# Kernel tuning notes

Measured on AMD Instinct MI355X. Metric: run time of the kernel, lower is better.

The kernel has to match this reference:

```python
import jax, jax.numpy as jnp
import numpy as np

T, H, E, I, K = 4096, 2048, 8, 1408, 2


def setup_inputs() -> dict:
    key = jax.random.key(0)
    k1, k2, k3, k4 = jax.random.split(key, 4)
    x = jax.random.normal(k1, (T, H), dtype=jnp.float32)
    router_w = jax.random.normal(k2, (H, E), dtype=jnp.float32) * 0.02
    gate_up_proj = jax.random.normal(k3, (E, H, 2 * I), dtype=jnp.float32) * 0.02
    down_proj = jax.random.normal(k4, (E, I, H), dtype=jnp.float32) * 0.02
    return {"x": x, "router_w": router_w, "gate_up_proj": gate_up_proj, "down_proj": down_proj}


def _moe_forward(x, router_w, gate_up_proj, down_proj):
    # --- Router: softmax over experts, top-k selection (Qwen2-MoE style) ---
    logits = x @ router_w                                  # [T, E]
    probs = jax.nn.softmax(logits, axis=-1)
    topk_w, topk_idx = jax.lax.top_k(probs, K)             # [T, K]

    # --- Permute: replicate tokens per selected expert, stable-sort by expert id ---
    flat_eid = topk_idx.reshape(-1)                        # [T*K]
    rep_x = jnp.repeat(x, K, axis=0)                       # [T*K, H]
    sort_idx = jnp.argsort(flat_eid, stable=True)          # token permute (like ops.permute)
    perm_x = rep_x[sort_idx]                               # [T*K, H] grouped by expert
    perm_eid = flat_eid[sort_idx]                          # [T*K]

    # --- Grouped expert MLP (gate_up GEMM -> SiLU*up -> down GEMM) ---
    # Faithful to grouped-GEMM math; expressed as a fixed loop over E experts
    # with row masking to stay jit-compatible (no data-dependent shapes).
    out = jnp.zeros_like(perm_x)
    for e in range(E):
        gu = perm_x @ gate_up_proj[e]                      # [T*K, 2I]
        gate, up = gu[:, :I], gu[:, I:]
        h = (jax.nn.silu(gate) * up) @ down_proj[e]        # [T*K, H]
        out = out + jnp.where((perm_eid == e)[:, None], h, 0.0)

    # --- Unpermute + weighted combine over top-k ---
    inv_sort = jnp.argsort(sort_idx)                       # inverse permute mapping
    unperm = out[inv_sort].reshape(T, K, H)
    return jnp.einsum('tkh,tk->th', unperm, topk_w)        # [T, H]


def reference(x, router_w, gate_up_proj, down_proj):
    return _moe_forward(x, router_w, gate_up_proj, down_proj)
```

## Files before the change

### kernel.cpp

```cpp
#include <hip/hip_runtime.h>
#include <hip/hip_bf16.h>

#define T_TOK 4096
#define H_DIM 2048
#define E_NUM 8
#define I_DIM 1408
#define RTOT  8192
#define N1DIM 2816
#define MAXMT 40
#define MAXROWS 10752
#define NT1   11
#define NKT1  64
#define NKT2  44
#define G1_BLOCKS 440
#define GU_TILES 11264
#define DN_BLOCKS 2816
#define RT_BLOCKS 1024

#define BUF1U 16384
#define LDS1  131072

typedef __bf16 bf16x8 __attribute__((ext_vector_type(8)));
typedef float  floatx4 __attribute__((ext_vector_type(4)));
typedef unsigned short ushortx8 __attribute__((ext_vector_type(8)));

#define VMCNT(n) asm volatile("s_waitcnt vmcnt(" #n ")" ::: "memory")
#define LGK0() do { asm volatile("s_waitcnt lgkmcnt(0)" ::: "memory"); __builtin_amdgcn_sched_barrier(0); } while(0)

__device__ __forceinline__ unsigned short f2bf(float f) {
  union { float f; unsigned u; } v; v.f = f;
  unsigned r = v.u + 0x7FFFu + ((v.u >> 16) & 1u);
  return (unsigned short)(r >> 16);
}

__device__ __forceinline__ void async16(const void* g, void* l) {
  __builtin_amdgcn_global_load_lds(
      (__attribute__((address_space(1))) void*)(g),
      (__attribute__((address_space(3))) void*)(l), 16, 0, 0);
}

__global__ void prep_kernel(const float* __restrict__ W, unsigned short* __restrict__ W1T,
                            const float* __restrict__ x, const float* __restrict__ rw,
                            int* __restrict__ topk_idx, float* __restrict__ topk_w,
                            int* __restrict__ counts) {
  __shared__ unsigned short t[64][72];
  int bid = blockIdx.x;
  if (bid < RT_BLOCKS) {
    int wave = threadIdx.x >> 6, lane = threadIdx.x & 63;
    int tk = bid * 4 + wave;
    const float* xr = x + (size_t)tk * H_DIM;
    float acc[E_NUM];
#pragma unroll
    for (int e = 0; e < E_NUM; e++) acc[e] = 0.f;
    for (int h = lane; h < H_DIM; h += 64) {
      float xv = xr[h];
      const float* wr = rw + h * E_NUM;
#pragma unroll
      for (int e = 0; e < E_NUM; e++) acc[e] += xv * wr[e];
    }
#pragma unroll
    for (int e = 0; e < E_NUM; e++) {
      float v = acc[e];
#pragma unroll
      for (int s = 32; s > 0; s >>= 1) v += __shfl_xor(v, s, 64);
      acc[e] = v;
    }
    if (lane == 0) {
      float mx = acc[0];
#pragma unroll
      for (int e = 1; e < E_NUM; e++) mx = fmaxf(mx, acc[e]);
      float p[E_NUM], s = 0.f;
#pragma unroll
      for (int e = 0; e < E_NUM; e++) { p[e] = __expf(acc[e] - mx); s += p[e]; }
      float inv = 1.0f / s;
      int i0 = 0;
#pragma unroll
      for (int e = 1; e < E_NUM; e++) if (p[e] > p[i0]) i0 = e;
      int i1 = (i0 == 0) ? 1 : 0;
#pragma unroll
      for (int e = 0; e < E_NUM; e++) if (e != i0 && p[e] > p[i1]) i1 = e;
      topk_idx[tk * 2]     = i0;
      topk_idx[tk * 2 + 1] = i1;
      topk_w[tk * 2]       = p[i0] * inv;
      topk_w[tk * 2 + 1]   = p[i1] * inv;
      atomicAdd(&counts[i0], 1);
      atomicAdd(&counts[i1], 1);
    }
    return;
  }
  int b = bid - RT_BLOCKS;
  int kt = b & 31;
  int j  = (b >> 5) % 44;
  int e  = b / (32 * 44);
  int f4 = threadIdx.x & 15, kr = threadIdx.x >> 4;
  int up = f4 >> 3, cc = (f4 & 7) * 4;
  int src_col = (up ? I_DIM : 0) + 32 * j + cc;
  int lrow = 32 * (cc >> 4) + 16 * up + (cc & 15);
  const float* src = W + ((size_t)e * H_DIM + (size_t)kt * 64) * (2 * I_DIM) + src_col;
#pragma unroll
  for (int p = 0; p < 4; p++) {
    int k = kr + p * 16;
    float4 v = *(const float4*)(src + (size_t)k * (2 * I_DIM));
    t[lrow + 0][k] = f2bf(v.x);
    t[lrow + 1][k] = f2bf(v.y);
    t[lrow + 2][k] = f2bf(v.z);
    t[lrow + 3][k] = f2bf(v.w);
  }
  __syncthreads();
  int c = threadIdx.x & 15, nr = threadIdx.x >> 4;
  unsigned short* Op = W1T + ((size_t)e * N1DIM + 64 * j) * H_DIM + kt * 64;
#pragma unroll
  for (int p = 0; p < 4; p++) {
    int n = nr + p * 16;
    *(ushort4*)(Op + (size_t)n * H_DIM + c * 4) = *(const ushort4*)&t[n][c * 4];
  }
}

__global__ void scan_kernel(const int* __restrict__ counts, int* __restrict__ cursors,
                            int* __restrict__ t1e, int* __restrict__ t1m0, int* __restrict__ t1end) {
  if (threadIdx.x == 0) {
    int o = 0, n1t = 0;
    for (int e = 0; e < E_NUM; e++) {
      int c = counts[e];
      cursors[e] = o;
      int n1 = (c + 255) >> 8;
      for (int j = 0; j < n1; j++) { t1e[n1t] = e; t1m0[n1t] = o + 256 * j; t1end[n1t] = o + c; n1t++; }
      o += 256 * n1;
    }
    for (; n1t < MAXMT; n1t++) t1e[n1t] = -1;
  }
}

__global__ void assign_kernel(const int* __restrict__ topk_idx, int* __restrict__ cursors,
                              int* __restrict__ row_of, int* __restrict__ tok_of) {
  int i = blockIdx.x * blockDim.x + threadIdx.x;
  int e = topk_idx[i];
  int row = atomicAdd(&cursors[e], 1);
  row_of[i] = row;
  tok_of[row] = i >> 1;
}

__global__ void gather_kernel(const float* __restrict__ x, const int* __restrict__ tok_of,
                              const int* __restrict__ t1e, const int* __restrict__ t1m0,
                              const int* __restrict__ t1end, unsigned short* __restrict__ Xp) {
  int mt = blockIdx.x >> 8;
  if (t1e[mt] < 0) return;
  int r = blockIdx.x & 255;
  int row = t1m0[mt] + r;
  int end = t1end[mt];
  int rr = row < end ? row : end - 1;
  int tok = tok_of[rr];
  const float4* src = (const float4*)(x + (size_t)tok * H_DIM);
  int i = threadIdx.x;
  float4 v0 = src[i * 2], v1 = src[i * 2 + 1];
  ushortx8 o;
  o[0] = f2bf(v0.x); o[1] = f2bf(v0.y); o[2] = f2bf(v0.z); o[3] = f2bf(v0.w);
  o[4] = f2bf(v1.x); o[5] = f2bf(v1.y); o[6] = f2bf(v1.z); o[7] = f2bf(v1.w);
  *(ushortx8*)(Xp + (size_t)row * H_DIM + i * 8) = o;
}

#define STG_A(lb) do { async16(gA0, (lb) + dA0); gA0 += 32; async16(gA1, (lb) + dA1); gA1 += 32; } while(0)
#define STG_B(lb) do { async16(gB0, (lb) + dB0); gB0 += 32; async16(gB1, (lb) + dB1); gB1 += 32; } while(0)

__global__ __launch_bounds__(512, 2) void gemm1_kernel(
    const unsigned short* __restrict__ Xp, const unsigned short* __restrict__ W1T,
    const float* __restrict__ Wdn, unsigned short* __restrict__ WdT,
    const int* __restrict__ t1e, const int* __restrict__ t1m0, const int* __restrict__ t1end,
    unsigned short* __restrict__ Hmid) {
  extern __shared__ unsigned short sm[];
  int bid = blockIdx.x;
  int tid = threadIdx.x;
  if (bid >= G1_BLOCKS) {
    int db = bid - G1_BLOCKS;
    int kt = db % 22;
    int nb = (db / 22) & 15;
    int e  = db / (22 * 16);
    int k0 = kt * 64, n0 = nb * 128;
    unsigned short (*t2)[72] = (unsigned short (*)[72])sm;
    int f4 = tid & 31, kr = tid >> 5;
    const float* src = Wdn + (size_t)e * I_DIM * H_DIM + (size_t)k0 * H_DIM + n0 + f4 * 4;
#pragma unroll
    for (int p = 0; p < 4; p++) {
      int k = kr + p * 16;
      float4 v = *(const float4*)(src + (size_t)k * H_DIM);
      t2[f4 * 4 + 0][k] = f2bf(v.x);
      t2[f4 * 4 + 1][k] = f2bf(v.y);
      t2[f4 * 4 + 2][k] = f2bf(v.z);
      t2[f4 * 4 + 3][k] = f2bf(v.w);
    }
    __syncthreads();
    int c = tid & 15, nr = tid >> 4;
#pragma unroll
    for (int p = 0; p < 4; p++) {
      int n = nr + p * 32;
      *(ushort4*)(WdT + ((size_t)e * H_DIM + n0 + n) * I_DIM + k0 + c * 4) = *(const ushort4*)&t2[n][c * 4];
    }
    return;
  }
  int xcd = bid & 7, jj = bid >> 3;
  int mt = xcd * 5 + jj / NT1, nt = jj % NT1;
  int e = t1e[mt];
  if (e < 0) return;
  int m0 = t1m0[mt], rend = t1end[mt];
  int n0 = nt * 256;
  int wave = tid >> 6, lane = tid & 63;
  int wm = wave >> 2, wn = wave & 3;
  int l15 = lane & 15, qq = lane >> 4;

  int u0 = wave * 128 + lane, u1 = u0 + 64;
  int r0 = u0 >> 2, s0 = (u0 & 3) ^ ((u0 >> 3) & 3);
  int r1 = u1 >> 2, s1 = (u1 & 3) ^ ((u1 >> 3) & 3);
  const unsigned short* gA0 = Xp + (size_t)(m0 + r0) * H_DIM + s0 * 8;
  const unsigned short* gA1 = Xp + (size_t)(m0 + r1) * H_DIM + s1 * 8;
  const unsigned short* gB0 = W1T + ((size_t)e * N1DIM + (n0 + r0)) * H_DIM + s0 * 8;
  const unsigned short* gB1 = W1T + ((size_t)e * N1DIM + (n0 + r1)) * H_DIM + s1 * 8;
  int dA0 = u0 * 8, dA1 = u1 * 8;
  int dB0 = 8192 + u0 * 8, dB1 = 8192 + u1 * 8;

  int sw = (qq ^ ((l15 >> 1) & 3)) * 16;
  int sA = (wm * 128 + l15) * 64 + sw;
  int sB = 16384 + (wn * 64 + l15) * 64 + sw;

  STG_A(sm); STG_B(sm);
  { unsigned short* lb = sm + BUF1U; STG_A(lb); STG_B(lb); }
  floatx4 acc[8][4] = {};
  VMCNT(4);
  __builtin_amdgcn_s_barrier();

  for (int t = 0; t < NKT1; t++) {
    const char* sb = (const char*)(sm + (t & 3) * BUF1U);
    unsigned short* lb = sm + ((t + 2) & 3) * BUF1U;
    bool pf = (t + 2 < NKT1);
    bf16x8 a[8], b0, b1, b2, b3;
#pragma unroll
    for (int fr = 0; fr < 8; fr++) a[fr] = *(const bf16x8*)(sb + sA + fr * 1024);
    b0 = *(const bf16x8*)(sb + sB);
    b1 = *(const bf16x8*)(sb + sB + 1024);
    if (pf) STG_A(lb);
    __builtin_amdgcn_s_barrier();
    LGK0();
    __builtin_amdgcn_s_setprio(1);
#pragma unroll
    for (int fr = 0; fr < 8; fr++) {
      acc[fr][0] = __builtin_amdgcn_mfma_f32_16x16x32_bf16(a[fr], b0, acc[fr][0], 0, 0, 0);
      acc[fr][1] = __builtin_amdgcn_mfma_f32_16x16x32_bf16(a[fr], b1, acc[fr][1], 0, 0, 0);
    }
    __builtin_amdgcn_s_setprio(0);
    __builtin_amdgcn_s_barrier();
    b2 = *(const bf16x8*)(sb + sB + 2048);
    b3 = *(const bf16x8*)(sb + sB + 3072);
    if (pf) { STG_B(lb); VMCNT(4); } else { VMCNT(0); }
    __builtin_amdgcn_s_barrier();
    LGK0();
    __builtin_amdgcn_s_setprio(1);
#pragma unroll
    for (int fr = 0; fr < 8; fr++) {
      acc[fr][2] = __builtin_amdgcn_mfma_f32_16x16x32_bf16(a[fr], b2, acc[fr][2], 0, 0, 0);
      acc[fr][3] = __builtin_amdgcn_mfma_f32_16x16x32_bf16(a[fr], b3, acc[fr][3], 0, 0, 0);
    }
    __builtin_amdgcn_s_setprio(0);
  }

  int rb = wm * 128 + (lane >> 4) * 4;
  int lc0 = nt * 128 + wn * 32 + l15;
#pragma unroll
  for (int fr = 0; fr < 8; fr++) {
#pragma unroll
    for (int p = 0; p < 2; p++) {
      int lcol = lc0 + p * 16;
#pragma unroll
      for (int r = 0; r < 4; r++) {
        int arow = m0 + rb + fr * 16 + r;
        if (arow < rend) {
          float g = acc[fr][2 * p][r];
          float u = acc[fr][2 * p + 1][r];
          float s = g / (1.0f + __expf(-g));
          Hmid[(size_t)arow * I_DIM + lcol] = f2bf(s * u);
        }
      }
    }
  }
}

__global__ __launch_bounds__(512, 2) void gemm2_kernel(
    const unsigned short* __restrict__ Hmid, const unsigned short* __restrict__ WdT,
    const int* __restrict__ t1e, const int* __restrict__ t1m0, const int* __restrict__ t1end,
    float* __restrict__ H2) {
  extern __shared__ unsigned short sm[];
  int bid = blockIdx.x;
  int xcd = bid & 7, jj = bid >> 3;
  int mt = xcd * 5 + (jj >> 3), nt = jj & 7;
  int e = t1e[mt];
  if (e < 0) return;
  int m0 = t1m0[mt], rend = t1end[mt];
  int n0 = nt * 256;
  int tid = threadIdx.x, wave = tid >> 6, lane = tid & 63;
  int wm = wave >> 2, wn = wave & 3;
  int l15 = lane & 15, qq = lane >> 4;

  int u0 = wave * 128 + lane, u1 = u0 + 64;
  int r0 = u0 >> 2, s0 = (u0 & 3) ^ ((u0 >> 3) & 3);
  int r1 = u1 >> 2, s1 = (u1 & 3) ^ ((u1 >> 3) & 3);
  const unsigned short* gA0 = Hmid + (size_t)(m0 + r0) * I_DIM + s0 * 8;
  const unsigned short* gA1 = Hmid + (size_t)(m0 + r1) * I_DIM + s1 * 8;
  const unsigned short* gB0 = WdT + ((size_t)e * H_DIM + (n0 + r0)) * I_DIM + s0 * 8;
  const unsigned short* gB1 = WdT + ((size_t)e * H_DIM + (n0 + r1)) * I_DIM + s1 * 8;
  int dA0 = u0 * 8, dA1 = u1 * 8;
  int dB0 = 8192 + u0 * 8, dB1 = 8192 + u1 * 8;

  int sw = (qq ^ ((l15 >> 1) & 3)) * 16;
  int sA = (wm * 128 + l15) * 64 + sw;
  int sB = 16384 + (wn * 64 + l15) * 64 + sw;

  STG_A(sm); STG_B(sm);
  { unsigned short* lb = sm + BUF1U; STG_A(lb); STG_B(lb); }
  floatx4 acc[8][4] = {};
  VMCNT(4);
  __builtin_amdgcn_s_barrier();

  for (int t = 0; t < NKT2; t++) {
    const char* sb = (const char*)(sm + (t & 3) * BUF1U);
    unsigned short* lb = sm + ((t + 2) & 3) * BUF1U;
    bool pf = (t + 2 < NKT2);
    bf16x8 a[8], b0, b1, b2, b3;
#pragma unroll
    for (int fr = 0; fr < 8; fr++) a[fr] = *(const bf16x8*)(sb + sA + fr * 1024);
    b0 = *(const bf16x8*)(sb + sB);
    b1 = *(const bf16x8*)(sb + sB + 1024);
    if (pf) STG_A(lb);
    __builtin_amdgcn_s_barrier();
    LGK0();
    __builtin_amdgcn_s_setprio(1);
#pragma unroll
    for (int fr = 0; fr < 8; fr++) {
      acc[fr][0] = __builtin_amdgcn_mfma_f32_16x16x32_bf16(a[fr], b0, acc[fr][0], 0, 0, 0);
      acc[fr][1] = __builtin_amdgcn_mfma_f32_16x16x32_bf16(a[fr], b1, acc[fr][1], 0, 0, 0);
    }
    __builtin_amdgcn_s_setprio(0);
    __builtin_amdgcn_s_barrier();
    b2 = *(const bf16x8*)(sb + sB + 2048);
    b3 = *(const bf16x8*)(sb + sB + 3072);
    if (pf) { STG_B(lb); VMCNT(4); } else { VMCNT(0); }
    __builtin_amdgcn_s_barrier();
    LGK0();
    __builtin_amdgcn_s_setprio(1);
#pragma unroll
    for (int fr = 0; fr < 8; fr++) {
      acc[fr][2] = __builtin_amdgcn_mfma_f32_16x16x32_bf16(a[fr], b2, acc[fr][2], 0, 0, 0);
      acc[fr][3] = __builtin_amdgcn_mfma_f32_16x16x32_bf16(a[fr], b3, acc[fr][3], 0, 0, 0);
    }
    __builtin_amdgcn_s_setprio(0);
  }

  int rb = wm * 128 + (lane >> 4) * 4;
  int cb = n0 + wn * 64 + l15;
#pragma unroll
  for (int fr = 0; fr < 8; fr++) {
#pragma unroll
    for (int ni = 0; ni < 4; ni++) {
#pragma unroll
      for (int r = 0; r < 4; r++) {
        int arow = m0 + rb + fr * 16 + r;
        if (arow < rend) H2[(size_t)arow * H_DIM + cb + ni * 16] = acc[fr][ni][r];
      }
    }
  }
}

__global__ void combine_kernel(const float* __restrict__ H2, const int* __restrict__ row_of,
                               const float* __restrict__ topk_w, float* __restrict__ out) {
  int t = blockIdx.x >> 1;
  int part = blockIdx.x & 1;
  int c = part * 1024 + threadIdx.x * 4;
  int r0 = row_of[t * 2], r1 = row_of[t * 2 + 1];
  float w0 = topk_w[t * 2], w1 = topk_w[t * 2 + 1];
  float4 a = *(const float4*)(H2 + (size_t)r0 * H_DIM + c);
  float4 b = *(const float4*)(H2 + (size_t)r1 * H_DIM + c);
  float4 o;
  o.x = w0 * a.x + w1 * b.x;
  o.y = w0 * a.y + w1 * b.y;
  o.z = w0 * a.z + w1 * b.z;
  o.w = w0 * a.w + w1 * b.w;
  *(float4*)(out + (size_t)t * H_DIM + c) = o;
}

extern "C" void kernel_launch(void* const* d_in, const int* in_sizes, int n_in,
                              void* d_out, int out_size, void* d_ws, size_t ws_size,
                              hipStream_t stream) {
  const float* x   = (const float*)d_in[0];
  const float* rw  = (const float*)d_in[1];
  const float* wgu = (const float*)d_in[2];
  const float* wdn = (const float*)d_in[3];
  float* out = (float*)d_out;

  static bool attr_done = false;
  if (!attr_done) {
    hipFuncSetAttribute(reinterpret_cast<const void*>(gemm1_kernel),
                        hipFuncAttributeMaxDynamicSharedMemorySize, LDS1);
    hipFuncSetAttribute(reinterpret_cast<const void*>(gemm2_kernel),
                        hipFuncAttributeMaxDynamicSharedMemorySize, LDS1);
    attr_done = true;
  }

  char* ws = (char*)d_ws;
  size_t off = 0;
  auto alloc = [&](size_t b) {
    char* p = ws + off;
    off = (off + b + 255) & ~(size_t)255;
    return p;
  };
  unsigned short* W1T  = (unsigned short*)alloc((size_t)E_NUM * N1DIM * H_DIM * 2);
  unsigned short* WdT  = (unsigned short*)alloc((size_t)E_NUM * H_DIM * I_DIM * 2);
  unsigned short* Xp   = (unsigned short*)alloc((size_t)MAXROWS * H_DIM * 2);
  unsigned short* Hmid = (unsigned short*)alloc((size_t)MAXROWS * I_DIM * 2);
  float* H2            = (float*)alloc((size_t)MAXROWS * H_DIM * 4);
  int*   topk_idx      = (int*)alloc(RTOT * 4);
  float* topk_w        = (float*)alloc(RTOT * 4);
  int*   row_of        = (int*)alloc(RTOT * 4);
  int*   tok_of        = (int*)alloc((size_t)MAXROWS * 4);
  int*   counts        = (int*)alloc(256);
  int*   cursors       = (int*)alloc(256);
  int*   t1e           = (int*)alloc(MAXMT * 4);
  int*   t1m0          = (int*)alloc(MAXMT * 4);
  int*   t1end         = (int*)alloc(MAXMT * 4);

  hipMemsetAsync(counts, 0, E_NUM * sizeof(int), stream);

  prep_kernel<<<RT_BLOCKS + GU_TILES, 256, 0, stream>>>(wgu, W1T, x, rw, topk_idx, topk_w, counts);
  scan_kernel<<<1, 64, 0, stream>>>(counts, cursors, t1e, t1m0, t1end);
  assign_kernel<<<RTOT / 256, 256, 0, stream>>>(topk_idx, cursors, row_of, tok_of);
  gather_kernel<<<MAXMT * 256, 256, 0, stream>>>(x, tok_of, t1e, t1m0, t1end, Xp);
  gemm1_kernel<<<G1_BLOCKS + DN_BLOCKS, 512, LDS1, stream>>>(Xp, W1T, wdn, WdT, t1e, t1m0, t1end, Hmid);
  gemm2_kernel<<<320, 512, LDS1, stream>>>(Hmid, WdT, t1e, t1m0, t1end, H2);
  combine_kernel<<<T_TOK * 2, 256, 0, stream>>>(H2, row_of, topk_w, out);
}
```

Baseline: 693.6 us.

## Store transposed bf16 weights in K-blocked layout with wider conversion tiles

The fp32-to-bf16 weight transposes for both the gate_up and down projections now write into a K-blocked layout: each 64-wide K slab is stored contiguously per expert. The GEMM B-operand loaders step through that layout with alternating increments. Each conversion block also handles a wider 256-column tile, reading full rows for better coalescing, so fewer blocks are launched. The goal is more contiguous weight reads and writes in both the conversion and GEMM stages, at the cost of more complex address arithmetic and a larger, possibly bank-conflicting LDS staging tile.

Measured after the change: 688.5 us. About the same (-0.7%).

```diff
diff --git a/kernel.cpp b/kernel.cpp
--- a/kernel.cpp
+++ b/kernel.cpp
@@ -13,9 +13,11 @@
 #define NKT1  64
 #define NKT2  44
 #define G1_BLOCKS 440
-#define GU_TILES 11264
-#define DN_BLOCKS 2816
+#define GU_BLOCKS 2816
+#define DN_BLOCKS 1408
 #define RT_BLOCKS 1024
+#define BLK1 180224
+#define BLK2 131072
 
 #define BUF1U 16384
 #define LDS1  131072
@@ -43,10 +45,11 @@
                             const float* __restrict__ x, const float* __restrict__ rw,
                             int* __restrict__ topk_idx, float* __restrict__ topk_w,
                             int* __restrict__ counts) {
-  __shared__ unsigned short t[64][72];
+  __shared__ unsigned short t[64][258];
   int bid = blockIdx.x;
+  int tid = threadIdx.x;
   if (bid < RT_BLOCKS) {
-    int wave = threadIdx.x >> 6, lane = threadIdx.x & 63;
+    int wave = tid >> 6, lane = tid & 63;
     int tk = bid * 4 + wave;
     const float* xr = x + (size_t)tk * H_DIM;
     float acc[E_NUM];
@@ -90,29 +93,37 @@
   }
   int b = bid - RT_BLOCKS;
   int kt = b & 31;
-  int j  = (b >> 5) % 44;
-  int e  = b / (32 * 44);
-  int f4 = threadIdx.x & 15, kr = threadIdx.x >> 4;
-  int up = f4 >> 3, cc = (f4 & 7) * 4;
-  int src_col = (up ? I_DIM : 0) + 32 * j + cc;
-  int lrow = 32 * (cc >> 4) + 16 * up + (cc & 15);
-  const float* src = W + ((size_t)e * H_DIM + (size_t)kt * 64) * (2 * I_DIM) + src_col;
-#pragma unroll
-  for (int p = 0; p < 4; p++) {
-    int k = kr + p * 16;
-    float4 v = *(const float4*)(src + (size_t)k * (2 * I_DIM));
-    t[lrow + 0][k] = f2bf(v.x);
-    t[lrow + 1][k] = f2bf(v.y);
-    t[lrow + 2][k] = f2bf(v.z);
-    t[lrow + 3][k] = f2bf(v.w);
+  int cw = (b >> 5) % 11;
+  int e  = b / (32 * 11);
+  int k0 = kt * 64, c0 = cw * 256;
+  int f = tid & 63, kw = tid >> 6;
+  const float* srcb = W + ((size_t)e * H_DIM + k0) * (2 * I_DIM) + c0 + f * 4;
+  float4 vv[16];
+#pragma unroll
+  for (int p = 0; p < 16; p++)
+    vv[p] = *(const float4*)(srcb + (size_t)(p * 4 + kw) * (2 * I_DIM));
+#pragma unroll
+  for (int p = 0; p < 16; p++) {
+    int k = p * 4 + kw;
+    ushort2 lo, hi;
+    lo.x = f2bf(vv[p].x); lo.y = f2bf(vv[p].y);
+    hi.x = f2bf(vv[p].z); hi.y = f2bf(vv[p].w);
+    *(ushort2*)&t[k][f * 4]     = lo;
+    *(ushort2*)&t[k][f * 4 + 2] = hi;
   }
   __syncthreads();
-  int c = threadIdx.x & 15, nr = threadIdx.x >> 4;
-  unsigned short* Op = W1T + ((size_t)e * N1DIM + 64 * j) * H_DIM + kt * 64;
-#pragma unroll
-  for (int p = 0; p < 4; p++) {
-    int n = nr + p * 16;
-    *(ushort4*)(Op + (size_t)n * H_DIM + c * 4) = *(const ushort4*)&t[n][c * 4];
+  int c = tid & 15, rg = tid >> 4;
+  unsigned short* Ob = W1T + ((size_t)e * 32 + kt) * BLK1;
+#pragma unroll
+  for (int p = 0; p < 16; p++) {
+    int rr = p * 16 + rg;
+    int sc = c0 + rr;
+    int np = (sc < I_DIM) ? (((sc >> 4) << 5) + (sc & 15))
+                          : ((((sc - I_DIM) >> 4) << 5) + 16 + ((sc - I_DIM) & 15));
+    ushort4 o;
+    o.x = t[c * 4 + 0][rr]; o.y = t[c * 4 + 1][rr];
+    o.z = t[c * 4 + 2][rr]; o.w = t[c * 4 + 3][rr];
+    *(ushort4*)(Ob + (size_t)np * 64 + c * 4) = o;
   }
 }
 
@@ -160,7 +171,7 @@
 }
 
 #define STG_A(lb) do { async16(gA0, (lb) + dA0); gA0 += 32; async16(gA1, (lb) + dA1); gA1 += 32; } while(0)
-#define STG_B(lb) do { async16(gB0, (lb) + dB0); gB0 += 32; async16(gB1, (lb) + dB1); gB1 += 32; } while(0)
+#define STG_B(lb, inc) do { async16(gB0, (lb) + dB0); gB0 += (inc); async16(gB1, (lb) + dB1); gB1 += (inc); } while(0)
 
 __global__ __launch_bounds__(512, 2) void gemm1_kernel(
     const unsigned short* __restrict__ Xp, const unsigned short* __restrict__ W1T,
@@ -173,27 +184,36 @@
   if (bid >= G1_BLOCKS) {
     int db = bid - G1_BLOCKS;
     int kt = db % 22;
-    int nb = (db / 22) & 15;
-    int e  = db / (22 * 16);
-    int k0 = kt * 64, n0 = nb * 128;
-    unsigned short (*t2)[72] = (unsigned short (*)[72])sm;
-    int f4 = tid & 31, kr = tid >> 5;
-    const float* src = Wdn + (size_t)e * I_DIM * H_DIM + (size_t)k0 * H_DIM + n0 + f4 * 4;
-#pragma unroll
-    for (int p = 0; p < 4; p++) {
-      int k = kr + p * 16;
-      float4 v = *(const float4*)(src + (size_t)k * H_DIM);
-      t2[f4 * 4 + 0][k] = f2bf(v.x);
-      t2[f4 * 4 + 1][k] = f2bf(v.y);
-      t2[f4 * 4 + 2][k] = f2bf(v.z);
-      t2[f4 * 4 + 3][k] = f2bf(v.w);
+    int nw = (db / 22) & 7;
+    int e  = db / (22 * 8);
+    int k0 = kt * 64, n0w = nw * 256;
+    unsigned short (*t2)[258] = (unsigned short (*)[258])sm;
+    int f = tid & 63, kw = tid >> 6;
+    const float* srcb = Wdn + (size_t)e * I_DIM * H_DIM + (size_t)k0 * H_DIM + n0w + f * 4;
+    float4 vv[8];
+#pragma unroll
+    for (int p = 0; p < 8; p++)
+      vv[p] = *(const float4*)(srcb + (size_t)(p * 8 + kw) * H_DIM);
+#pragma unroll
+    for (int p = 0; p < 8; p++) {
+      int k = p * 8 + kw;
+      ushort2 lo, hi;
+      lo.x = f2bf(vv[p].x); lo.y = f2bf(vv[p].y);
+      hi.x = f2bf(vv[p].z); hi.y = f2bf(vv[p].w);
+      *(ushort2*)&t2[k][f * 4]     = lo;
+      *(ushort2*)&t2[k][f * 4 + 2] = hi;
     }
     __syncthreads();
-    int c = tid & 15, nr = tid >> 4;
-#pragma unroll
-    for (int p = 0; p < 4; p++) {
-      int n = nr + p * 32;
-      *(ushort4*)(WdT + ((size_t)e * H_DIM + n0 + n) * I_DIM + k0 + c * 4) = *(const ushort4*)&t2[n][c * 4];
+    int c = tid & 15, rg = tid >> 4;
+    unsigned short* Ob = WdT + ((size_t)e * 22 + kt) * BLK2;
+#pragma unroll
+    for (int p = 0; p < 8; p++) {
+      int rr = p * 32 + rg;
+      int n = n0w + rr;
+      ushort4 o;
+      o.x = t2[c * 4 + 0][rr]; o.y = t2[c * 4 + 1][rr];
+      o.z = t2[c * 4 + 2][rr]; o.w = t2[c * 4 + 3][rr];
+      *(ushort4*)(Ob + (size_t)n * 64 + c * 4) = o;
     }
     return;
   }
@@ -212,8 +232,8 @@
   int r1 = u1 >> 2, s1 = (u1 & 3) ^ ((u1 >> 3) & 3);
   const unsigned short* gA0 = Xp + (size_t)(m0 + r0) * H_DIM + s0 * 8;
   const unsigned short* gA1 = Xp + (size_t)(m0 + r1) * H_DIM + s1 * 8;
-  const unsigned short* gB0 = W1T + ((size_t)e * N1DIM + (n0 + r0)) * H_DIM + s0 * 8;
-  const unsigned short* gB1 = W1T + ((size_t)e * N1DIM + (n0 + r1)) * H_DIM + s1 * 8;
+  const unsigned short* gB0 = W1T + (size_t)e * N1DIM * H_DIM + (size_t)(n0 + r0) * 64 + s0 * 8;
+  const unsigned short* gB1 = W1T + (size_t)e * N1DIM * H_DIM + (size_t)(n0 + r1) * 64 + s1 * 8;
   int dA0 = u0 * 8, dA1 = u1 * 8;
   int dB0 = 8192 + u0 * 8, dB1 = 8192 + u1 * 8;
 
@@ -221,8 +241,8 @@
   int sA = (wm * 128 + l15) * 64 + sw;
   int sB = 16384 + (wn * 64 + l15) * 64 + sw;
 
-  STG_A(sm); STG_B(sm);
-  { unsigned short* lb = sm + BUF1U; STG_A(lb); STG_B(lb); }
+  STG_A(sm); STG_B(sm, 32);
+  { unsigned short* lb = sm + BUF1U; STG_A(lb); STG_B(lb, BLK1 - 32); }
   floatx4 acc[8][4] = {};
   VMCNT(4);
   __builtin_amdgcn_s_barrier();
@@ -249,7 +269,7 @@
     __builtin_amdgcn_s_barrier();
     b2 = *(const bf16x8*)(sb + sB + 2048);
     b3 = *(const bf16x8*)(sb + sB + 3072);
-    if (pf) { STG_B(lb); VMCNT(4); } else { VMCNT(0); }
+    if (pf) { STG_B(lb, (t & 1) ? (BLK1 - 32) : 32); VMCNT(4); } else { VMCNT(0); }
     __builtin_amdgcn_s_barrier();
     LGK0();
     __builtin_amdgcn_s_setprio(1);
@@ -303,8 +323,8 @@
   int r1 = u1 >> 2, s1 = (u1 & 3) ^ ((u1 >> 3) & 3);
   const unsigned short* gA0 = Hmid + (size_t)(m0 + r0) * I_DIM + s0 * 8;
   const unsigned short* gA1 = Hmid + (size_t)(m0 + r1) * I_DIM + s1 * 8;
-  const unsigned short* gB0 = WdT + ((size_t)e * H_DIM + (n0 + r0)) * I_DIM + s0 * 8;
-  const unsigned short* gB1 = WdT + ((size_t)e * H_DIM + (n0 + r1)) * I_DIM + s1 * 8;
+  const unsigned short* gB0 = WdT + (size_t)e * H_DIM * I_DIM + (size_t)(n0 + r0) * 64 + s0 * 8;
+  const unsigned short* gB1 = WdT + (size_t)e * H_DIM * I_DIM + (size_t)(n0 + r1) * 64 + s1 * 8;
   int dA0 = u0 * 8, dA1 = u1 * 8;
   int dB0 = 8192 + u0 * 8, dB1 = 8192 + u1 * 8;
 
@@ -312,8 +332,8 @@
   int sA = (wm * 128 + l15) * 64 + sw;
   int sB = 16384 + (wn * 64 + l15) * 64 + sw;
 
-  STG_A(sm); STG_B(sm);
-  { unsigned short* lb = sm + BUF1U; STG_A(lb); STG_B(lb); }
+  STG_A(sm); STG_B(sm, 32);
+  { unsigned short* lb = sm + BUF1U; STG_A(lb); STG_B(lb, BLK2 - 32); }
   floatx4 acc[8][4] = {};
   VMCNT(4);
   __builtin_amdgcn_s_barrier();
@@ -340,7 +360,7 @@
     __builtin_amdgcn_s_barrier();
     b2 = *(const bf16x8*)(sb + sB + 2048);
     b3 = *(const bf16x8*)(sb + sB + 3072);
-    if (pf) { STG_B(lb); VMCNT(4); } else { VMCNT(0); }
+    if (pf) { STG_B(lb, (t & 1) ? (BLK2 - 32) : 32); VMCNT(4); } else { VMCNT(0); }
     __builtin_amdgcn_s_barrier();
     LGK0();
     __builtin_amdgcn_s_setprio(1);
@@ -426,7 +446,7 @@
 
   hipMemsetAsync(counts, 0, E_NUM * sizeof(int), stream);
 
-  prep_kernel<<<RT_BLOCKS + GU_TILES, 256, 0, stream>>>(wgu, W1T, x, rw, topk_idx, topk_w, counts);
+  prep_kernel<<<RT_BLOCKS + GU_BLOCKS, 256, 0, stream>>>(wgu, W1T, x, rw, topk_idx, topk_w, counts);
   scan_kernel<<<1, 64, 0, stream>>>(counts, cursors, t1e, t1m0, t1end);
   assign_kernel<<<RTOT / 256, 256, 0, stream>>>(topk_idx, cursors, row_of, tok_of);
   gather_kernel<<<MAXMT * 256, 256, 0, stream>>>(x, tok_of, t1e, t1m0, t1end, Xp);
```
